# Performance work log

Measured on AMD Instinct MI355X. Metric: run time of the kernel, lower is better.

Reference implementation:

```python
import jax, jax.numpy as jnp
import numpy as np


def _discretize(A, B, C, step):
    # Bilinear (Tustin) discretization, as in the source module.
    N = A.shape[0]
    I = jnp.eye(N, dtype=A.dtype)
    BL = jnp.linalg.inv(I - (step / 2.0) * A)
    Ab = BL @ (I + (step / 2.0) * A)
    Bb = (BL * step) @ B  # (N, 1)
    return Ab, Bb, C


def _k_conv(Ab, Bb, Cb, L):
    # K[l] = Cb @ Ab^l @ Bb, computed by a linear recurrence instead of
    # L explicit matrix powers (same math as the source's K_conv).
    def step(v, _):
        k = (Cb @ v)[0, 0]
        return Ab @ v, k

    _, K = jax.lax.scan(step, Bb, None, length=L)
    return K  # (L,)


def setup_inputs() -> dict:
    key = jax.random.key(0)
    k_u, k_a, k_b, k_c, k_s = jax.random.split(key, 5)
    N, L, BATCH = 64, 16384, 512
    u = jax.random.normal(k_u, (BATCH, L), dtype=jnp.float32)
    # lecun_normal inits: std = 1/sqrt(fan_in)
    A = jax.random.normal(k_a, (N, N), dtype=jnp.float32) / np.sqrt(N)
    B = jax.random.normal(k_b, (N, 1), dtype=jnp.float32)  # fan_in = 1
    C = jax.random.normal(k_c, (1, N), dtype=jnp.float32) / np.sqrt(N)
    D = jnp.ones((1,), dtype=jnp.float32)
    # log_step_initializer(dt_min=1e-3, dt_max=0.1)
    lo, hi = np.log(1e-3), np.log(0.1)
    log_step = (jax.random.uniform(k_s, (1,)) * (hi - lo) + lo).astype(jnp.float32)
    return {"u": u, "A": A, "B": B, "C": C, "D": D, "log_step": log_step}


def reference(u, A, B, C, D, log_step) -> jnp.ndarray:
    L = u.shape[-1]
    step = jnp.exp(log_step)  # (1,)
    Ab, Bb, Cb = _discretize(A, B, C, step)
    K = _k_conv(Ab, Bb, Cb, L)  # (L,)
    # FFT causal convolution: pad both signals to length 2L (as in source),
    # multiply in frequency domain, take first L samples.
    n = 2 * L
    ud = jnp.fft.rfft(u, n=n, axis=-1)          # (BATCH, L+1) complex
    Kd = jnp.fft.rfft(K, n=n)                   # (L+1,) complex, broadcast
    y = jnp.fft.irfft(ud * Kd, n=n, axis=-1)[..., :L]
    return y + D * u
```

## Files before the change

kernel.cpp:

```cpp
#include <hip/hip_runtime.h>
#include <cstddef>

typedef double f64x4 __attribute__((ext_vector_type(4)));
typedef float  f32x4 __attribute__((ext_vector_type(4)));
typedef short  bf16x8 __attribute__((ext_vector_type(8)));

static constexpr int RCN = 512 * 128;

static constexpr size_t WS_W  = 0;
static constexpr size_t WS_G  = 8192;
static constexpr size_t WS_MD = 32768;
static constexpr size_t WS_BV = 40960;
static constexpr size_t WS_X  = WS_BV + (size_t)RCN * 64;

__device__ __forceinline__ unsigned short f2bf(float f) {
  union { float f; unsigned u; } v; v.f = f;
  unsigned u = v.u + 0x7FFFu + ((v.u >> 16) & 1u);
  return (unsigned short)(u >> 16);
}

__device__ __forceinline__ double probeE(int i, int k) {
  return (double)(((i * 3 + k * 5) & 7) - 3);
}
__device__ __forceinline__ double probeF(int k, int j) {
  return (double)(((k * 7 + j * 2) & 7) - 4);
}

__device__ __forceinline__ bool probe_mfma_layout(int lr, int lq, int rowm[4], int* colm_out)
{
  f64x4 z; z[0] = 0.0; z[1] = 0.0; z[2] = 0.0; z[3] = 0.0;
  f64x4 p1 = __builtin_amdgcn_mfma_f64_16x16x4f64((double)lr, 1.0, z, 0, 0, 0);
  f64x4 p2 = __builtin_amdgcn_mfma_f64_16x16x4f64(1.0, (double)lr, z, 0, 0, 0);
  bool okl = true;
#pragma unroll
  for (int r = 0; r < 4; ++r) {
    int rr = (int)(p1[r] * 0.25 + 0.5);
    okl = okl && (p1[r] == 4.0 * (double)rr) && rr >= 0 && rr < 16;
    rowm[r] = rr & 15;
    okl = okl && (p2[r] == p2[0]);
  }
  int cc = (int)(p2[0] * 0.25 + 0.5);
  okl = okl && (p2[0] == 4.0 * (double)cc) && cc >= 0 && cc < 16;
  *colm_out = cc & 15;
  f64x4 d = __builtin_amdgcn_mfma_f64_16x16x4f64(probeE(lr, lq), probeF(lq, lr), z, 0, 0, 0);
#pragma unroll
  for (int r = 0; r < 4; ++r) {
    double ref = 0.0;
#pragma unroll
    for (int k = 0; k < 4; ++k) ref += probeE(rowm[r], k) * probeF(k, cc & 15);
    okl = okl && (d[r] == ref);
  }
  return __all(okl) != 0;
}

template<bool ADD>
__device__ __forceinline__ void mm64_mfma(const double* A, const double* B, double* D,
                                          int wi, int wj, int lr, int lq,
                                          const int rowm[4], int colm)
{
  f64x4 acc;
  if (ADD) {
#pragma unroll
    for (int r = 0; r < 4; ++r)
      acc[r] = D[(wi * 16 + rowm[r]) * 65 + wj * 16 + colm];
  } else {
    acc[0] = 0.0; acc[1] = 0.0; acc[2] = 0.0; acc[3] = 0.0;
  }
#pragma unroll
  for (int kb = 0; kb < 16; ++kb) {
    double a = A[(wi * 16 + lr) * 65 + kb * 4 + lq];
    double b = B[(kb * 4 + lq) * 65 + wj * 16 + lr];
    acc = __builtin_amdgcn_mfma_f64_16x16x4f64(a, b, acc, 0, 0, 0);
  }
  __syncthreads();
#pragma unroll
  for (int r = 0; r < 4; ++r)
    D[(wi * 16 + rowm[r]) * 65 + wj * 16 + colm] = acc[r];
  __syncthreads();
}

__device__ __forceinline__ void wh_tile(const float* Wf, const float* Hf,
                                        const double* Pd, float* Wo, float* Ho,
                                        int n, bool isW, int wi, int wj,
                                        int lr, int lq, const int rowm[4], int colm)
{
  f64x4 acc;
  acc[0] = 0.0; acc[1] = 0.0; acc[2] = 0.0; acc[3] = 0.0;
#pragma unroll
  for (int kb = 0; kb < 16; ++kb) {
    double a, b;
    if (isW) {
      a = (double)Wf[(wi * 16 + lr) * 65 + kb * 4 + lq];
      b = Pd[(wj * 16 + lr) * 65 + kb * 4 + lq];
    } else {
      a = (double)Hf[(wi * 16 + lr) * 65 + kb * 4 + lq];
      b = Pd[(kb * 4 + lq) * 65 + wj * 16 + lr];
    }
    acc = __builtin_amdgcn_mfma_f64_16x16x4f64(a, b, acc, 0, 0, 0);
  }
#pragma unroll
  for (int r = 0; r < 4; ++r) {
    int drow = wi * 16 + rowm[r];
    if (drow < n) {
      if (isW) Wo[(n + drow) * 65 + wj * 16 + colm] = (float)acc[r];
      else     Ho[(n + drow) * 65 + wj * 16 + colm] = (float)acc[r];
    }
  }
}

template<bool ADD>
__device__ __forceinline__ void mm64x2(const double* A, const double* B, double* D,
                                       int tr2, int tc2)
{
  double a00 = 0, a01 = 0, a10 = 0, a11 = 0;
#pragma unroll 8
  for (int c = 0; c < 64; ++c) {
    double av0 = A[(tr2 + 0) * 65 + c];
    double av1 = A[(tr2 + 1) * 65 + c];
    double bv0 = B[c * 65 + tc2 + 0];
    double bv1 = B[c * 65 + tc2 + 1];
    a00 = fma(av0, bv0, a00); a01 = fma(av0, bv1, a01);
    a10 = fma(av1, bv0, a10); a11 = fma(av1, bv1, a11);
  }
  double o00, o01, o10, o11;
  if (ADD) {
    o00 = D[(tr2 + 0) * 65 + tc2 + 0]; o01 = D[(tr2 + 0) * 65 + tc2 + 1];
    o10 = D[(tr2 + 1) * 65 + tc2 + 0]; o11 = D[(tr2 + 1) * 65 + tc2 + 1];
  }
  __syncthreads();
  D[(tr2 + 0) * 65 + tc2 + 0] = ADD ? (o00 + a00) : a00;
  D[(tr2 + 0) * 65 + tc2 + 1] = ADD ? (o01 + a01) : a01;
  D[(tr2 + 1) * 65 + tc2 + 0] = ADD ? (o10 + a10) : a10;
  D[(tr2 + 1) * 65 + tc2 + 1] = ADD ? (o11 + a11) : a11;
  __syncthreads();
}

__global__ __launch_bounds__(1024) void k_precomp(
    const float* __restrict__ Ain, const float* __restrict__ Bin,
    const float* __restrict__ Cin, const float* __restrict__ Din,
    const float* __restrict__ LS, float* ws)
{
  __shared__ double Xd[64 * 65];
  __shared__ double Pd[64 * 65];
  __shared__ float  Wf[128 * 65];
  __shared__ float  Hf[128 * 65];
  __shared__ float  Kf[128];

  const int t    = threadIdx.x;
  const int wave = t >> 6;
  const int lane = t & 63;
  const int lr   = lane & 15;
  const int lq   = lane >> 4;
  const int wv_i = wave >> 2;
  const int wv_j = wave & 3;
  const int tr2  = (t >> 5) << 1;
  const int tc2  = (t & 31) << 1;

  int rowm[4]; int colm;
  const bool use_mfma = probe_mfma_layout(lr, lq, rowm, &colm);

  unsigned short* Wtg = (unsigned short*)(ws + WS_W);
  unsigned short* Gtg = (unsigned short*)(ws + WS_G);
  float* Mf = ws + WS_MD;

  const double step = exp((double)LS[0]);
  const double h = 0.5 * step;

  for (int idx = t; idx < 4096; idx += 1024) {
    int i = idx >> 6, j = idx & 63;
    double a = h * (double)Ain[idx];
    Xd[i * 65 + j] = a;
    Pd[i * 65 + j] = a + ((i == j) ? 1.0 : 0.0);
  }
  __syncthreads();

  if (use_mfma) {
    for (int k = 0; k < 3; ++k) {
      mm64_mfma<false>(Xd, Xd, Xd, wv_i, wv_j, lr, lq, rowm, colm);
      mm64_mfma<true >(Pd, Xd, Pd, wv_i, wv_j, lr, lq, rowm, colm);
    }
  } else {
    for (int k = 0; k < 3; ++k) {
      mm64x2<false>(Xd, Xd, Xd, tr2, tc2);
      mm64x2<true >(Pd, Xd, Pd, tr2, tc2);
    }
  }

  if (t < 64) {
    double bb = 0.0;
    for (int c = 0; c < 64; ++c) bb = fma(Pd[t * 65 + c], (double)Bin[c], bb);
    Wf[t] = (float)(bb * step);
  }
  __syncthreads();

  for (int idx = t; idx < 4096; idx += 1024) {
    int i = idx >> 6, j = idx & 63;
    Pd[i * 65 + j] = 2.0 * Pd[i * 65 + j] - ((i == j) ? 1.0 : 0.0);
  }
  __syncthreads();

  if (t < 64) {
    double hh = 0.0;
    for (int c = 0; c < 64; ++c) hh = fma((double)Cin[c], Pd[c * 65 + t], hh);
    Hf[t] = (float)hh;
  }
  __syncthreads();

  if (use_mfma) {
    for (int k = 0; k < 7; ++k) {
      const int n     = 1 << k;
      const int tpm   = (n + 15) >> 4;
      const int tiles = tpm << 2;
      if (tiles <= 8) {
        if (wave < 2 * tiles) {
          const bool isW = wave < tiles;
          const int  w   = isW ? wave : wave - tiles;
          wh_tile(Wf, Hf, Pd, Wf, Hf, n, isW, w >> 2, w & 3, lr, lq, rowm, colm);
        }
      } else {
        wh_tile(Wf, Hf, Pd, Wf, Hf, n, true,  wv_i, wv_j, lr, lq, rowm, colm);
        wh_tile(Wf, Hf, Pd, Wf, Hf, n, false, wv_i, wv_j, lr, lq, rowm, colm);
      }
      mm64_mfma<false>(Pd, Pd, Pd, wv_i, wv_j, lr, lq, rowm, colm);
    }
  } else {
    for (int k = 0; k < 7; ++k) {
      const int n = 1 << k;
      if (n <= 16) {
        if (t < (n << 6)) {
          int r = t >> 6, ii = t & 63;
          double aw = 0.0, ah = 0.0;
#pragma unroll 4
          for (int c = 0; c < 64; ++c) {
            aw = fma(Pd[ii * 65 + c], (double)Wf[r * 65 + c], aw);
            ah = fma((double)Hf[r * 65 + c], Pd[c * 65 + ii], ah);
          }
          Wf[(n + r) * 65 + ii] = (float)aw;
          Hf[(n + r) * 65 + ii] = (float)ah;
        }
      } else if (n == 32) {
        const int r  = t >> 5;
        const int i2 = (t & 31) << 1;
        double w0 = 0, w1 = 0, h0 = 0, h1 = 0;
#pragma unroll 4
        for (int c = 0; c < 64; ++c) {
          double wr = (double)Wf[r * 65 + c];
          w0 = fma(wr, Pd[(i2 + 0) * 65 + c], w0);
          w1 = fma(wr, Pd[(i2 + 1) * 65 + c], w1);
          double hr = (double)Hf[r * 65 + c];
          h0 = fma(hr, Pd[c * 65 + i2 + 0], h0);
          h1 = fma(hr, Pd[c * 65 + i2 + 1], h1);
        }
        Wf[(32 + r) * 65 + i2 + 0] = (float)w0;
        Wf[(32 + r) * 65 + i2 + 1] = (float)w1;
        Hf[(32 + r) * 65 + i2 + 0] = (float)h0;
        Hf[(32 + r) * 65 + i2 + 1] = (float)h1;
      } else {
        const int r2 = tr2, i2 = tc2;
        double w00 = 0, w01 = 0, w10 = 0, w11 = 0;
        double h00 = 0, h01 = 0, h10 = 0, h11 = 0;
#pragma unroll 4
        for (int c = 0; c < 64; ++c) {
          double wa = (double)Wf[(r2 + 0) * 65 + c];
          double wb = (double)Wf[(r2 + 1) * 65 + c];
          double p0 = Pd[(i2 + 0) * 65 + c];
          double p1 = Pd[(i2 + 1) * 65 + c];
          w00 = fma(wa, p0, w00); w01 = fma(wa, p1, w01);
          w10 = fma(wb, p0, w10); w11 = fma(wb, p1, w11);
          double ha = (double)Hf[(r2 + 0) * 65 + c];
          double hb = (double)Hf[(r2 + 1) * 65 + c];
          double q0 = Pd[c * 65 + i2 + 0];
          double q1 = Pd[c * 65 + i2 + 1];
          h00 = fma(ha, q0, h00); h01 = fma(ha, q1, h01);
          h10 = fma(hb, q0, h10); h11 = fma(hb, q1, h11);
        }
        Wf[(64 + r2 + 0) * 65 + i2 + 0] = (float)w00;
        Wf[(64 + r2 + 0) * 65 + i2 + 1] = (float)w01;
        Wf[(64 + r2 + 1) * 65 + i2 + 0] = (float)w10;
        Wf[(64 + r2 + 1) * 65 + i2 + 1] = (float)w11;
        Hf[(64 + r2 + 0) * 65 + i2 + 0] = (float)h00;
        Hf[(64 + r2 + 0) * 65 + i2 + 1] = (float)h01;
        Hf[(64 + r2 + 1) * 65 + i2 + 0] = (float)h10;
        Hf[(64 + r2 + 1) * 65 + i2 + 1] = (float)h11;
      }
      mm64x2<false>(Pd, Pd, Pd, tr2, tc2);
    }
  }

  for (int idx = t; idx < 4096; idx += 1024)
    Mf[idx] = (float)Pd[(idx >> 6) * 65 + (idx & 63)];

  if (use_mfma) mm64_mfma<false>(Pd, Pd, Pd, wv_i, wv_j, lr, lq, rowm, colm);
  else          mm64x2<false>(Pd, Pd, Pd, tr2, tc2);
  for (int idx = t; idx < 4096; idx += 1024)
    Mf[4096 + idx] = (float)Pd[(idx >> 6) * 65 + (idx & 63)];

  if (t < 128) {
    double s = 0.0;
    for (int c = 0; c < 64; ++c) s = fma((double)Cin[c], (double)Wf[t * 65 + c], s);
    Kf[t] = (float)s;
  }
  __syncthreads();

  for (int idx = t; idx < 8192; idx += 1024) {
    int i = idx >> 7, kk = idx & 127;
    Wtg[idx] = f2bf(Wf[(127 - kk) * 65 + i]);
  }

  const float Dval = Din[0];
  for (int idx = t; idx < 16384; idx += 1024) {
    int r = idx >> 7, kg = idx & 127;
    float v = (r >= kg) ? Kf[r - kg] : 0.f;
    if (kg == r) v += Dval;
    Gtg[r * 192 + kg] = f2bf(v);
  }
  for (int idx = t; idx < 8192; idx += 1024) {
    int r = idx >> 6, i = idx & 63;
    Gtg[r * 192 + 128 + i] = f2bf(Hf[r * 65 + i]);
  }
}

__global__ __launch_bounds__(256, 2) void k_fused(
    const float* __restrict__ u, const unsigned short* __restrict__ Wt,
    const unsigned short* __restrict__ Gt, const float* __restrict__ Mf,
    float* __restrict__ out)
{
  __shared__ __align__(16) unsigned char Lds[78848];
  float*          bs  = (float*)(Lds);
  unsigned short* WtS = (unsigned short*)(Lds + 34816);
  float*          dsb = (float*)(Lds + 34816);
  unsigned short* Gs  = (unsigned short*)(Lds);
  unsigned short* As  = (unsigned short*)(Lds + 52224);
  float*          xs  = (float*)(Lds + 62464);
  unsigned short* Xbf = (unsigned short*)(Lds + 62464);

  const int t    = threadIdx.x;
  const int w    = t >> 6;
  const int lane = t & 63;
  const int lr   = lane & 15, lq = lane >> 4;
  const int row  = blockIdx.x;
  const float* urow = u + ((size_t)row << 14);
  float* orow = out + ((size_t)row << 14);

  auto stageA = [&](int k0) {
    for (int it = t; it < 1024; it += 256) {
      int rcl = it >> 3, k4 = (it & 7) << 2;
      float4 v = *(const float4*)&urow[(rcl << 7) + k0 + k4];
      ushort4 s;
      s.x = f2bf(v.x); s.y = f2bf(v.y); s.z = f2bf(v.z); s.w = f2bf(v.w);
      *(ushort4*)&As[rcl * 40 + k4] = s;
    }
  };

  {
    const unsigned* srcW = (const unsigned*)Wt;
    unsigned* dstW = (unsigned*)WtS;
    for (int idx = t; idx < 4096; idx += 256) {
      int r = idx >> 6, c = idx & 63;
      dstW[r * 68 + c] = srcW[idx];
    }
    stageA(0);
    __syncthreads();

    f32x4 acc[2][4];
#pragma unroll
    for (int i = 0; i < 2; ++i)
#pragma unroll
      for (int j = 0; j < 4; ++j) { acc[i][j][0] = 0.f; acc[i][j][1] = 0.f; acc[i][j][2] = 0.f; acc[i][j][3] = 0.f; }

    for (int sl = 0; sl < 4; ++sl) {
      bf16x8 av[2], bv[4];
#pragma unroll
      for (int ti = 0; ti < 2; ++ti)
        av[ti] = *(const bf16x8*)&As[(w * 32 + ti * 16 + lr) * 40 + lq * 8];
#pragma unroll
      for (int tj = 0; tj < 4; ++tj)
        bv[tj] = *(const bf16x8*)&WtS[(tj * 16 + lr) * 136 + sl * 32 + lq * 8];
#pragma unroll
      for (int ti = 0; ti < 2; ++ti)
#pragma unroll
        for (int tj = 0; tj < 4; ++tj)
          acc[ti][tj] = __builtin_amdgcn_mfma_f32_16x16x32_bf16(av[ti], bv[tj], acc[ti][tj], 0, 0, 0);
      if (sl < 3) {
        __syncthreads();
        stageA((sl + 1) << 5);
        __syncthreads();
      }
    }
#pragma unroll
    for (int ti = 0; ti < 2; ++ti)
#pragma unroll
      for (int tj = 0; tj < 4; ++tj)
#pragma unroll
        for (int r = 0; r < 4; ++r)
          bs[(w * 32 + ti * 16 + lq * 4 + r) * 68 + tj * 16 + lr] = acc[ti][tj][r];
    __syncthreads();
  }

  {
    float Mr[64];
#pragma unroll
    for (int c4 = 0; c4 < 16; ++c4)
      *(float4*)&Mr[c4 * 4] = *(const float4*)&Mf[(lane << 6) + c4 * 4];

    for (int k = 0; k < 16; ++k) {
      const int tp = (w << 4) + k;
      float y0 = 0.f, y1 = 0.f, y2 = 0.f, y3 = 0.f;
#pragma unroll
      for (int c4 = 0; c4 < 16; ++c4) {
        float4 bb = *(const float4*)&bs[(tp << 1) * 68 + (c4 << 2)];
        y0 = fmaf(Mr[c4 * 4 + 0], bb.x, y0);
        y1 = fmaf(Mr[c4 * 4 + 1], bb.y, y1);
        y2 = fmaf(Mr[c4 * 4 + 2], bb.z, y2);
        y3 = fmaf(Mr[c4 * 4 + 3], bb.w, y3);
      }
      dsb[tp * 68 + lane] = ((y0 + y1) + (y2 + y3)) + bs[((tp << 1) + 1) * 68 + lane];
    }
    __syncthreads();

    if (w == 0) {
      float M2r[64];
#pragma unroll
      for (int c4 = 0; c4 < 16; ++c4)
        *(float4*)&M2r[c4 * 4] = *(const float4*)&Mf[4096 + (lane << 6) + c4 * 4];
      float x = 0.f;
      float ecur = dsb[lane];
      for (int u2 = 0; u2 < 64; ++u2) {
        xs[(u2 << 6) + lane] = x;
        float en = (u2 < 63) ? dsb[(u2 + 1) * 68 + lane] : 0.f;
        const unsigned xb = __float_as_uint(x);
        float y0 = 0.f, y1 = 0.f, y2 = 0.f, y3 = 0.f;
#pragma unroll
        for (int c = 0; c < 64; c += 4) {
          y0 = fmaf(M2r[c + 0], __uint_as_float(__builtin_amdgcn_readlane(xb, c + 0)), y0);
          y1 = fmaf(M2r[c + 1], __uint_as_float(__builtin_amdgcn_readlane(xb, c + 1)), y1);
          y2 = fmaf(M2r[c + 2], __uint_as_float(__builtin_amdgcn_readlane(xb, c + 2)), y2);
          y3 = fmaf(M2r[c + 3], __uint_as_float(__builtin_amdgcn_readlane(xb, c + 3)), y3);
        }
        x = ((y0 + y1) + (y2 + y3)) + ecur;
        ecur = en;
      }
    }
    __syncthreads();

    for (int k = 0; k < 16; ++k) {
      const int tp = (w << 4) + k;
      float y0 = 0.f, y1 = 0.f, y2 = 0.f, y3 = 0.f;
#pragma unroll
      for (int c4 = 0; c4 < 16; ++c4) {
        float4 xx = *(const float4*)&xs[(tp << 6) + (c4 << 2)];
        y0 = fmaf(Mr[c4 * 4 + 0], xx.x, y0);
        y1 = fmaf(Mr[c4 * 4 + 1], xx.y, y1);
        y2 = fmaf(Mr[c4 * 4 + 2], xx.z, y2);
        y3 = fmaf(Mr[c4 * 4 + 3], xx.w, y3);
      }
      float xeven = xs[(tp << 6) + lane];
      float xodd  = ((y0 + y1) + (y2 + y3)) + bs[(tp << 1) * 68 + lane];
      Xbf[((tp << 1) + 0) * 64 + lane] = f2bf(xeven);
      Xbf[((tp << 1) + 1) * 64 + lane] = f2bf(xodd);
    }
    __syncthreads();
  }

  {
    const unsigned* srcG = (const unsigned*)Gt;
    unsigned* dstG = (unsigned*)Gs;
    for (int idx = t; idx < 12288; idx += 256) {
      int r = idx / 96, c = idx - r * 96;
      dstG[r * 100 + c] = srcG[idx];
    }
    stageA(0);
    __syncthreads();

    f32x4 acc[2][8];
#pragma unroll
    for (int i = 0; i < 2; ++i)
#pragma unroll
      for (int j = 0; j < 8; ++j) { acc[i][j][0] = 0.f; acc[i][j][1] = 0.f; acc[i][j][2] = 0.f; acc[i][j][3] = 0.f; }

    for (int sl = 0; sl < 6; ++sl) {
      bf16x8 av[2], bv[8];
#pragma unroll
      for (int ti = 0; ti < 2; ++ti) {
        if (sl < 4)
          av[ti] = *(const bf16x8*)&As[(w * 32 + ti * 16 + lr) * 40 + lq * 8];
        else
          av[ti] = *(const bf16x8*)&Xbf[(w * 32 + ti * 16 + lr) * 64 + (sl - 4) * 32 + lq * 8];
      }
#pragma unroll
      for (int tj = 0; tj < 8; ++tj)
        bv[tj] = *(const bf16x8*)&Gs[(tj * 16 + lr) * 200 + sl * 32 + lq * 8];
#pragma unroll
      for (int ti = 0; ti < 2; ++ti)
#pragma unroll
        for (int tj = 0; tj < 8; ++tj)
          acc[ti][tj] = __builtin_amdgcn_mfma_f32_16x16x32_bf16(av[ti], bv[tj], acc[ti][tj], 0, 0, 0);
      if (sl < 3) {
        __syncthreads();
        stageA((sl + 1) << 5);
        __syncthreads();
      }
    }

#pragma unroll
    for (int ti = 0; ti < 2; ++ti)
#pragma unroll
      for (int tj = 0; tj < 8; ++tj)
#pragma unroll
        for (int r = 0; r < 4; ++r) {
          int rcl = w * 32 + ti * 16 + lq * 4 + r;
          orow[((size_t)rcl << 7) + tj * 16 + lr] = acc[ti][tj][r];
        }
  }
}

extern "C" void kernel_launch(void* const* d_in, const int* in_sizes, int n_in,
                              void* d_out, int out_size, void* d_ws, size_t ws_size,
                              hipStream_t stream) {
  (void)in_sizes; (void)n_in; (void)out_size; (void)ws_size;
  const float* u  = (const float*)d_in[0];
  const float* A  = (const float*)d_in[1];
  const float* Bv = (const float*)d_in[2];
  const float* Cv = (const float*)d_in[3];
  const float* Dv = (const float*)d_in[4];
  const float* ls = (const float*)d_in[5];
  float* out = (float*)d_out;
  float* ws  = (float*)d_ws;

  k_precomp<<<1, 1024, 0, stream>>>(A, Bv, Cv, Dv, ls, ws);
  k_fused<<<512, 256, 0, stream>>>(u, (const unsigned short*)(ws + WS_W),
                                   (const unsigned short*)(ws + WS_G),
                                   ws + WS_MD, out);
}
```

Before: 188.6 us.

## Double-buffer precompute matmuls, interleave M layout, hoist M loads and A staging

The precompute kernel now ping-pongs between four shared buffers, so each 64x64 matmul writes to a separate output. This removes the extra barrier pair inside every matmul, and the VALU fallback is simplified. The M matrices are stored in an interleaved layout so each lane's float4 loads in the main kernel are coalesced. The Mr loads and the next stageA call are moved earlier so they overlap with other work. This costs more shared memory in precompute and changes several buffer lifetimes, so ordering mistakes are a risk.

After: 186.5 us. No clear change (-1.1%).

```diff
diff --git a/kernel.cpp b/kernel.cpp
--- a/kernel.cpp
+++ b/kernel.cpp
@@ -10,8 +10,6 @@
 static constexpr size_t WS_W  = 0;
 static constexpr size_t WS_G  = 8192;
 static constexpr size_t WS_MD = 32768;
-static constexpr size_t WS_BV = 40960;
-static constexpr size_t WS_X  = WS_BV + (size_t)RCN * 64;
 
 __device__ __forceinline__ unsigned short f2bf(float f) {
   union { float f; unsigned u; } v; v.f = f;
@@ -53,16 +51,16 @@
   return __all(okl) != 0;
 }
 
-template<bool ADD>
-__device__ __forceinline__ void mm64_mfma(const double* A, const double* B, double* D,
+__device__ __forceinline__ void mmPP_mfma(const double* A, const double* B,
+                                          const double* Cin, double* D,
                                           int wi, int wj, int lr, int lq,
                                           const int rowm[4], int colm)
 {
   f64x4 acc;
-  if (ADD) {
+  if (Cin) {
 #pragma unroll
     for (int r = 0; r < 4; ++r)
-      acc[r] = D[(wi * 16 + rowm[r]) * 65 + wj * 16 + colm];
+      acc[r] = Cin[(wi * 16 + rowm[r]) * 65 + wj * 16 + colm];
   } else {
     acc[0] = 0.0; acc[1] = 0.0; acc[2] = 0.0; acc[3] = 0.0;
   }
@@ -72,11 +70,33 @@
     double b = B[(kb * 4 + lq) * 65 + wj * 16 + lr];
     acc = __builtin_amdgcn_mfma_f64_16x16x4f64(a, b, acc, 0, 0, 0);
   }
-  __syncthreads();
 #pragma unroll
   for (int r = 0; r < 4; ++r)
     D[(wi * 16 + rowm[r]) * 65 + wj * 16 + colm] = acc[r];
-  __syncthreads();
+}
+
+__device__ __forceinline__ void mmPP_valu(const double* A, const double* B,
+                                          const double* Cin, double* D,
+                                          int tr2, int tc2)
+{
+  double a00, a01, a10, a11;
+  if (Cin) {
+    a00 = Cin[(tr2 + 0) * 65 + tc2 + 0]; a01 = Cin[(tr2 + 0) * 65 + tc2 + 1];
+    a10 = Cin[(tr2 + 1) * 65 + tc2 + 0]; a11 = Cin[(tr2 + 1) * 65 + tc2 + 1];
+  } else { a00 = a01 = a10 = a11 = 0.0; }
+#pragma unroll 8
+  for (int c = 0; c < 64; ++c) {
+    double av0 = A[(tr2 + 0) * 65 + c];
+    double av1 = A[(tr2 + 1) * 65 + c];
+    double bv0 = B[c * 65 + tc2 + 0];
+    double bv1 = B[c * 65 + tc2 + 1];
+    a00 = fma(av0, bv0, a00); a01 = fma(av0, bv1, a01);
+    a10 = fma(av1, bv0, a10); a11 = fma(av1, bv1, a11);
+  }
+  D[(tr2 + 0) * 65 + tc2 + 0] = a00;
+  D[(tr2 + 0) * 65 + tc2 + 1] = a01;
+  D[(tr2 + 1) * 65 + tc2 + 0] = a10;
+  D[(tr2 + 1) * 65 + tc2 + 1] = a11;
 }
 
 __device__ __forceinline__ void wh_tile(const float* Wf, const float* Hf,
@@ -108,43 +128,18 @@
   }
 }
 
-template<bool ADD>
-__device__ __forceinline__ void mm64x2(const double* A, const double* B, double* D,
-                                       int tr2, int tc2)
-{
-  double a00 = 0, a01 = 0, a10 = 0, a11 = 0;
-#pragma unroll 8
-  for (int c = 0; c < 64; ++c) {
-    double av0 = A[(tr2 + 0) * 65 + c];
-    double av1 = A[(tr2 + 1) * 65 + c];
-    double bv0 = B[c * 65 + tc2 + 0];
-    double bv1 = B[c * 65 + tc2 + 1];
-    a00 = fma(av0, bv0, a00); a01 = fma(av0, bv1, a01);
-    a10 = fma(av1, bv0, a10); a11 = fma(av1, bv1, a11);
-  }
-  double o00, o01, o10, o11;
-  if (ADD) {
-    o00 = D[(tr2 + 0) * 65 + tc2 + 0]; o01 = D[(tr2 + 0) * 65 + tc2 + 1];
-    o10 = D[(tr2 + 1) * 65 + tc2 + 0]; o11 = D[(tr2 + 1) * 65 + tc2 + 1];
-  }
-  __syncthreads();
-  D[(tr2 + 0) * 65 + tc2 + 0] = ADD ? (o00 + a00) : a00;
-  D[(tr2 + 0) * 65 + tc2 + 1] = ADD ? (o01 + a01) : a01;
-  D[(tr2 + 1) * 65 + tc2 + 0] = ADD ? (o10 + a10) : a10;
-  D[(tr2 + 1) * 65 + tc2 + 1] = ADD ? (o11 + a11) : a11;
-  __syncthreads();
-}
-
 __global__ __launch_bounds__(1024) void k_precomp(
     const float* __restrict__ Ain, const float* __restrict__ Bin,
     const float* __restrict__ Cin, const float* __restrict__ Din,
     const float* __restrict__ LS, float* ws)
 {
-  __shared__ double Xd[64 * 65];
-  __shared__ double Pd[64 * 65];
-  __shared__ float  Wf[128 * 65];
-  __shared__ float  Hf[128 * 65];
+  __shared__ double SB0[64 * 65];
+  __shared__ double SB1[64 * 65];
+  __shared__ double SB2[64 * 65];
+  __shared__ double SB3[64 * 65];
   __shared__ float  Kf[128];
+  float* Wf = (float*)SB0;
+  float* Hf = (float*)SB1;
 
   const int t    = threadIdx.x;
   const int wave = t >> 6;
@@ -169,131 +164,91 @@
   for (int idx = t; idx < 4096; idx += 1024) {
     int i = idx >> 6, j = idx & 63;
     double a = h * (double)Ain[idx];
-    Xd[i * 65 + j] = a;
-    Pd[i * 65 + j] = a + ((i == j) ? 1.0 : 0.0);
+    SB0[i * 65 + j] = a;
+    SB2[i * 65 + j] = a + ((i == j) ? 1.0 : 0.0);
   }
   __syncthreads();
 
-  if (use_mfma) {
+  {
+    double *Xc = SB0, *Xn = SB1, *Zc = SB2, *Zn = SB3;
     for (int k = 0; k < 3; ++k) {
-      mm64_mfma<false>(Xd, Xd, Xd, wv_i, wv_j, lr, lq, rowm, colm);
-      mm64_mfma<true >(Pd, Xd, Pd, wv_i, wv_j, lr, lq, rowm, colm);
-    }
-  } else {
-    for (int k = 0; k < 3; ++k) {
-      mm64x2<false>(Xd, Xd, Xd, tr2, tc2);
-      mm64x2<true >(Pd, Xd, Pd, tr2, tc2);
+      if (use_mfma) mmPP_mfma(Xc, Xc, nullptr, Xn, wv_i, wv_j, lr, lq, rowm, colm);
+      else          mmPP_valu(Xc, Xc, nullptr, Xn, tr2, tc2);
+      __syncthreads();
+      if (use_mfma) mmPP_mfma(Zc, Xn, Zc, Zn, wv_i, wv_j, lr, lq, rowm, colm);
+      else          mmPP_valu(Zc, Xn, Zc, Zn, tr2, tc2);
+      __syncthreads();
+      double* tp_;
+      tp_ = Xc; Xc = Xn; Xn = tp_;
+      tp_ = Zc; Zc = Zn; Zn = tp_;
     }
   }
 
   if (t < 64) {
     double bb = 0.0;
-    for (int c = 0; c < 64; ++c) bb = fma(Pd[t * 65 + c], (double)Bin[c], bb);
+    for (int c = 0; c < 64; ++c) bb = fma(SB3[t * 65 + c], (double)Bin[c], bb);
     Wf[t] = (float)(bb * step);
   }
-  __syncthreads();
-
   for (int idx = t; idx < 4096; idx += 1024) {
     int i = idx >> 6, j = idx & 63;
-    Pd[i * 65 + j] = 2.0 * Pd[i * 65 + j] - ((i == j) ? 1.0 : 0.0);
+    SB2[i * 65 + j] = 2.0 * SB3[i * 65 + j] - ((i == j) ? 1.0 : 0.0);
   }
   __syncthreads();
 
   if (t < 64) {
     double hh = 0.0;
-    for (int c = 0; c < 64; ++c) hh = fma((double)Cin[c], Pd[c * 65 + t], hh);
+    for (int c = 0; c < 64; ++c) hh = fma((double)Cin[c], SB2[c * 65 + t], hh);
     Hf[t] = (float)hh;
   }
   __syncthreads();
 
-  if (use_mfma) {
-    for (int k = 0; k < 7; ++k) {
-      const int n     = 1 << k;
+  double* Pc = SB2;
+  double* Pn = SB3;
+  for (int k = 0; k < 7; ++k) {
+    const int n = 1 << k;
+    if (use_mfma) {
       const int tpm   = (n + 15) >> 4;
       const int tiles = tpm << 2;
       if (tiles <= 8) {
         if (wave < 2 * tiles) {
           const bool isW = wave < tiles;
-          const int  w   = isW ? wave : wave - tiles;
-          wh_tile(Wf, Hf, Pd, Wf, Hf, n, isW, w >> 2, w & 3, lr, lq, rowm, colm);
+          const int  wq  = isW ? wave : wave - tiles;
+          wh_tile(Wf, Hf, Pc, Wf, Hf, n, isW, wq >> 2, wq & 3, lr, lq, rowm, colm);
         }
       } else {
-        wh_tile(Wf, Hf, Pd, Wf, Hf, n, true,  wv_i, wv_j, lr, lq, rowm, colm);
-        wh_tile(Wf, Hf, Pd, Wf, Hf, n, false, wv_i, wv_j, lr, lq, rowm, colm);
-      }
-      mm64_mfma<false>(Pd, Pd, Pd, wv_i, wv_j, lr, lq, rowm, colm);
-    }
-  } else {
-    for (int k = 0; k < 7; ++k) {
-      const int n = 1 << k;
-      if (n <= 16) {
-        if (t < (n << 6)) {
-          int r = t >> 6, ii = t & 63;
-          double aw = 0.0, ah = 0.0;
-#pragma unroll 4
-          for (int c = 0; c < 64; ++c) {
-            aw = fma(Pd[ii * 65 + c], (double)Wf[r * 65 + c], aw);
-            ah = fma((double)Hf[r * 65 + c], Pd[c * 65 + ii], ah);
-          }
-          Wf[(n + r) * 65 + ii] = (float)aw;
-          Hf[(n + r) * 65 + ii] = (float)ah;
-        }
-      } else if (n == 32) {
-        const int r  = t >> 5;
-        const int i2 = (t & 31) << 1;
-        double w0 = 0, w1 = 0, h0 = 0, h1 = 0;
+        wh_tile(Wf, Hf, Pc, Wf, Hf, n, true,  wv_i, wv_j, lr, lq, rowm, colm);
+        wh_tile(Wf, Hf, Pc, Wf, Hf, n, false, wv_i, wv_j, lr, lq, rowm, colm);
+      }
+      mmPP_mfma(Pc, Pc, nullptr, Pn, wv_i, wv_j, lr, lq, rowm, colm);
+    } else {
+      for (int o = t; o < (n << 6); o += 1024) {
+        int r = o >> 6, ii = o & 63;
+        double aw = 0.0, ah = 0.0;
 #pragma unroll 4
         for (int c = 0; c < 64; ++c) {
-          double wr = (double)Wf[r * 65 + c];
-          w0 = fma(wr, Pd[(i2 + 0) * 65 + c], w0);
-          w1 = fma(wr, Pd[(i2 + 1) * 65 + c], w1);
-          double hr = (double)Hf[r * 65 + c];
-          h0 = fma(hr, Pd[c * 65 + i2 + 0], h0);
-          h1 = fma(hr, Pd[c * 65 + i2 + 1], h1);
+          aw = fma(Pc[ii * 65 + c], (double)Wf[r * 65 + c], aw);
+          ah = fma((double)Hf[r * 65 + c], Pc[c * 65 + ii], ah);
         }
-        Wf[(32 + r) * 65 + i2 + 0] = (float)w0;
-        Wf[(32 + r) * 65 + i2 + 1] = (float)w1;
-        Hf[(32 + r) * 65 + i2 + 0] = (float)h0;
-        Hf[(32 + r) * 65 + i2 + 1] = (float)h1;
-      } else {
-        const int r2 = tr2, i2 = tc2;
-        double w00 = 0, w01 = 0, w10 = 0, w11 = 0;
-        double h00 = 0, h01 = 0, h10 = 0, h11 = 0;
-#pragma unroll 4
-        for (int c = 0; c < 64; ++c) {
-          double wa = (double)Wf[(r2 + 0) * 65 + c];
-          double wb = (double)Wf[(r2 + 1) * 65 + c];
-          double p0 = Pd[(i2 + 0) * 65 + c];
-          double p1 = Pd[(i2 + 1) * 65 + c];
-          w00 = fma(wa, p0, w00); w01 = fma(wa, p1, w01);
-          w10 = fma(wb, p0, w10); w11 = fma(wb, p1, w11);
-          double ha = (double)Hf[(r2 + 0) * 65 + c];
-          double hb = (double)Hf[(r2 + 1) * 65 + c];
-          double q0 = Pd[c * 65 + i2 + 0];
-          double q1 = Pd[c * 65 + i2 + 1];
-          h00 = fma(ha, q0, h00); h01 = fma(ha, q1, h01);
-          h10 = fma(hb, q0, h10); h11 = fma(hb, q1, h11);
-        }
-        Wf[(64 + r2 + 0) * 65 + i2 + 0] = (float)w00;
-        Wf[(64 + r2 + 0) * 65 + i2 + 1] = (float)w01;
-        Wf[(64 + r2 + 1) * 65 + i2 + 0] = (float)w10;
-        Wf[(64 + r2 + 1) * 65 + i2 + 1] = (float)w11;
-        Hf[(64 + r2 + 0) * 65 + i2 + 0] = (float)h00;
-        Hf[(64 + r2 + 0) * 65 + i2 + 1] = (float)h01;
-        Hf[(64 + r2 + 1) * 65 + i2 + 0] = (float)h10;
-        Hf[(64 + r2 + 1) * 65 + i2 + 1] = (float)h11;
-      }
-      mm64x2<false>(Pd, Pd, Pd, tr2, tc2);
-    }
-  }
-
-  for (int idx = t; idx < 4096; idx += 1024)
-    Mf[idx] = (float)Pd[(idx >> 6) * 65 + (idx & 63)];
-
-  if (use_mfma) mm64_mfma<false>(Pd, Pd, Pd, wv_i, wv_j, lr, lq, rowm, colm);
-  else          mm64x2<false>(Pd, Pd, Pd, tr2, tc2);
-  for (int idx = t; idx < 4096; idx += 1024)
-    Mf[4096 + idx] = (float)Pd[(idx >> 6) * 65 + (idx & 63)];
+        Wf[(n + r) * 65 + ii] = (float)aw;
+        Hf[(n + r) * 65 + ii] = (float)ah;
+      }
+      mmPP_valu(Pc, Pc, nullptr, Pn, tr2, tc2);
+    }
+    __syncthreads();
+    double* tp_ = Pc; Pc = Pn; Pn = tp_;
+  }
+
+  for (int idx = t; idx < 4096; idx += 1024) {
+    int row = idx >> 6, col = idx & 63;
+    Mf[((col >> 2) << 8) + (row << 2) + (col & 3)] = (float)Pc[row * 65 + col];
+  }
+  if (use_mfma) mmPP_mfma(Pc, Pc, nullptr, Pn, wv_i, wv_j, lr, lq, rowm, colm);
+  else          mmPP_valu(Pc, Pc, nullptr, Pn, tr2, tc2);
+  __syncthreads();
+  for (int idx = t; idx < 4096; idx += 1024) {
+    int row = idx >> 6, col = idx & 63;
+    Mf[4096 + ((col >> 2) << 8) + (row << 2) + (col & 3)] = (float)Pn[row * 65 + col];
+  }
 
   if (t < 128) {
     double s = 0.0;
@@ -306,7 +261,6 @@
     int i = idx >> 7, kk = idx & 127;
     Wtg[idx] = f2bf(Wf[(127 - kk) * 65 + i]);
   }
-
   const float Dval = Din[0];
   for (int idx = t; idx < 16384; idx += 1024) {
     int r = idx >> 7, kg = idx & 127;
@@ -342,6 +296,11 @@
   const float* urow = u + ((size_t)row << 14);
   float* orow = out + ((size_t)row << 14);
 
+  float Mr[64];
+#pragma unroll
+  for (int c4 = 0; c4 < 16; ++c4)
+    *(float4*)&Mr[c4 * 4] = *(const float4*)&Mf[(c4 << 8) + (lane << 2)];
+
   auto stageA = [&](int k0) {
     for (int it = t; it < 1024; it += 256) {
       int rcl = it >> 3, k4 = (it & 7) << 2;
@@ -398,10 +357,7 @@
   }
 
   {
-    float Mr[64];
-#pragma unroll
-    for (int c4 = 0; c4 < 16; ++c4)
-      *(float4*)&Mr[c4 * 4] = *(const float4*)&Mf[(lane << 6) + c4 * 4];
+    stageA(0);
 
     for (int k = 0; k < 16; ++k) {
       const int tp = (w << 4) + k;
@@ -422,7 +378,7 @@
       float M2r[64];
 #pragma unroll
       for (int c4 = 0; c4 < 16; ++c4)
-        *(float4*)&M2r[c4 * 4] = *(const float4*)&Mf[4096 + (lane << 6) + c4 * 4];
+        *(float4*)&M2r[c4 * 4] = *(const float4*)&Mf[4096 + (c4 << 8) + (lane << 2)];
       float x = 0.f;
       float ecur = dsb[lane];
       for (int u2 = 0; u2 < 64; ++u2) {
@@ -469,7 +425,6 @@
       int r = idx / 96, c = idx - r * 96;
       dstG[r * 100 + c] = srcG[idx];
     }
-    stageA(0);
     __syncthreads();
 
     f32x4 acc[2][8];
```
